# Optimization experiments

Hardware: AMD Instinct MI355X
Metric: run time of the kernel (lower is better)

The kernel has to match this reference:

```python
import jax, jax.numpy as jnp
import numpy as np

D_MODEL = 1024
N_HEADS = 16
D_KV = 64
INNER = N_HEADS * D_KV
NUM_BUCKETS = 32
MAX_DISTANCE = 128
B, S = 4, 2048


def _relative_position_bucket(relative_position):
    # Mirrors T5Attention._relative_position_bucket (bidirectional variant)
    num_buckets = NUM_BUCKETS // 2  # 16
    relative_buckets = (relative_position > 0).astype(jnp.int32) * num_buckets
    rp = jnp.abs(relative_position)
    max_exact = num_buckets // 2  # 8
    is_small = rp < max_exact
    # clamp to 1 before log to avoid -inf (masked out by where anyway)
    rp_large = max_exact + (
        jnp.log(jnp.maximum(rp, 1).astype(jnp.float32) / max_exact)
        / np.log(MAX_DISTANCE / max_exact)
        * (num_buckets - max_exact)
    ).astype(jnp.int32)
    rp_large = jnp.minimum(rp_large, num_buckets - 1)
    return relative_buckets + jnp.where(is_small, rp.astype(jnp.int32), rp_large)


def setup_inputs() -> dict:
    key = jax.random.key(0)
    k1, k2, k3, k4, k5, k6 = jax.random.split(key, 6)
    hidden_states = jax.random.normal(k1, (B, S, D_MODEL), dtype=jnp.float32)
    positions = jnp.arange(B * S, dtype=jnp.int64 if jax.config.jax_enable_x64 else jnp.int32).reshape(B, S)
    mask = jnp.ones((B, S), dtype=jnp.float32)
    sc = 1.0 / np.sqrt(D_MODEL)
    wq = jax.random.normal(k2, (INNER, D_MODEL), dtype=jnp.float32) * sc
    wk = jax.random.normal(k3, (INNER, D_MODEL), dtype=jnp.float32) * sc
    wv = jax.random.normal(k4, (INNER, D_MODEL), dtype=jnp.float32) * sc
    wo = jax.random.normal(k5, (D_MODEL, INNER), dtype=jnp.float32) * sc
    rel_bias = jax.random.normal(k6, (NUM_BUCKETS, N_HEADS), dtype=jnp.float32)
    return {"hidden_states": hidden_states, "positions": positions, "mask": mask,
            "wq": wq, "wk": wk, "wv": wv, "wo": wo, "rel_bias": rel_bias}


def reference(hidden_states, positions, mask, wq, wk, wv, wo, rel_bias):
    Bq, Sq, _ = hidden_states.shape

    def shape_heads(x):  # [B,S,inner] -> [B,H,S,dkv]
        return x.reshape(Bq, Sq, N_HEADS, D_KV).transpose(0, 2, 1, 3)

    # position bias: [B,H,Sq,Sk]
    rel_pos = positions[:, None, :] - positions[:, :, None]  # memory - context
    buckets = _relative_position_bucket(rel_pos)             # [B,Sq,Sk]
    position_bias = rel_bias[buckets].transpose(0, 3, 1, 2)  # [B,H,Sq,Sk]

    q = shape_heads(hidden_states @ wq.T).astype(jnp.float32)
    k = shape_heads(hidden_states @ wk.T).astype(jnp.float32)
    v = shape_heads(hidden_states @ wv.T).astype(jnp.float32)

    scores = jnp.einsum('bhqd,bhkd->bhqk', q, k)  # no 1/sqrt(d) scaling (T5)
    bias = position_bias - 1000.0 * (1.0 - mask[:, None, None, :])
    attn = jax.nn.softmax(scores + bias, axis=-1)  # dropout p=0

    ctx = jnp.einsum('bhqk,bhkd->bhqd', attn, v)
    ctx = ctx.transpose(0, 2, 1, 3).reshape(Bq, Sq, INNER).astype(hidden_states.dtype)
    return ctx @ wo.T
```

## Files before the change

kernel.cpp:

```cpp
#include <hip/hip_runtime.h>
#include <cstdint>
#include <cstddef>

#define D_MODEL 1024
#define N_HEADS 16
#define INNER   1024
#define NBATCH  4
#define SEQ     2048
#define MTOT    (NBATCH * SEQ)
#define LOG2E   1.44269504088896f
#define BSTRIDE 4352
#define MASKC   1442.695041f

typedef _Float16 f16;
typedef __attribute__((ext_vector_type(8))) _Float16 f16x8;
typedef __attribute__((ext_vector_type(4))) _Float16 f16x4;
typedef __attribute__((ext_vector_type(2))) _Float16 f16x2;
typedef __attribute__((ext_vector_type(2))) __fp16   h16x2;
typedef __attribute__((ext_vector_type(4))) float    f32x4;

__device__ __forceinline__ f16x2 cvtpk(float x, float y) {
#if __has_builtin(__builtin_amdgcn_cvt_pkrtz)
  h16x2 r = __builtin_amdgcn_cvt_pkrtz(x, y);
  return __builtin_bit_cast(f16x2, r);
#else
  f16x2 r; r[0] = (f16)x; r[1] = (f16)y; return r;
#endif
}
__device__ __forceinline__ float dot2acc(f16x2 p, float acc) {
#if __has_builtin(__builtin_amdgcn_fdot2)
  h16x2 a = __builtin_bit_cast(h16x2, p);
  h16x2 one; one[0] = (__fp16)1.0f; one[1] = (__fp16)1.0f;
  return __builtin_amdgcn_fdot2(a, one, acc, false);
#else
  return acc + (float)p[0] + (float)p[1];
#endif
}

__global__ void k_cvt(const float* __restrict__ src, f16* __restrict__ dst, int n4, float scale) {
  int i = blockIdx.x * 256 + threadIdx.x;
  if (i < n4) {
    const float4 v = reinterpret_cast<const float4*>(src)[i];
    f16x4 h;
    h[0] = (f16)(v.x * scale); h[1] = (f16)(v.y * scale);
    h[2] = (f16)(v.z * scale); h[3] = (f16)(v.w * scale);
    reinterpret_cast<f16x4*>(dst)[i] = h;
  }
}

__global__ void k_cvtw(const float* __restrict__ wq, const float* __restrict__ wk,
                       const float* __restrict__ wv, const float* __restrict__ wo,
                       f16* __restrict__ dq, f16* __restrict__ dk,
                       f16* __restrict__ dv, f16* __restrict__ dwo) {
  const int y = blockIdx.y;
  const float* src = y == 0 ? wq : (y == 1 ? wk : (y == 2 ? wv : wo));
  f16* dst = y == 0 ? dq : (y == 1 ? dk : (y == 2 ? dv : dwo));
  const float scale = y == 0 ? LOG2E : 1.0f;
  const int i = blockIdx.x * 256 + threadIdx.x;
  const float4 v = reinterpret_cast<const float4*>(src)[i];
  f16x4 h;
  h[0] = (f16)(v.x * scale); h[1] = (f16)(v.y * scale);
  h[2] = (f16)(v.z * scale); h[3] = (f16)(v.w * scale);
  reinterpret_cast<f16x4*>(dst)[i] = h;
}

__global__ void k_bias(const float* __restrict__ relb, float* __restrict__ biasG) {
  const int i = blockIdx.x * 256 + threadIdx.x;
  const int h = blockIdx.y;
  const int d = i - 2048;
  const int sgn = d > 0 ? 16 : 0;
  const int a = d < 0 ? -d : d;
  int bucket;
  if (a < 8) {
    bucket = a;
  } else {
    float t = logf((float)a / 8.0f);
    t = t / 2.772588722239781f;
    t = t * 8.0f;
    int lg = 8 + (int)t;
    bucket = lg < 15 ? lg : 15;
  }
  biasG[h * BSTRIDE + i] = relb[(sgn + bucket) * N_HEADS + h] * LOG2E - MASKC;
}

__device__ __forceinline__ void gload_lds16(const void* g, void* l) {
  __builtin_amdgcn_global_load_lds(
      (const __attribute__((address_space(1))) unsigned int*)g,
      (__attribute__((address_space(3))) unsigned int*)l,
      16, 0, 0);
}

template <int MODE>
__device__ __forceinline__ void gemm_body(const f16* __restrict__ A,
                                          const f16* __restrict__ W,
                                          void* __restrict__ Cp,
                                          int m0, int n0) {
  __shared__ __align__(16) f16 As[128 * 64];
  __shared__ __align__(16) f16 Bs[128 * 64];
  const int t = threadIdx.x;
  const int lane = t & 63;
  const int wid = t >> 6;
  const int wr = wid >> 1;
  const int wc = wid & 1;
  const int g = lane >> 4;
  const int lr = lane & 15;

  f32x4 acc[4][4] = {};
  const char* Ab = (const char*)A;
  const char* Wb = (const char*)W;

  for (int kt = 0; kt < D_MODEL / 64; ++kt) {
    const int k0 = kt * 64;
    __syncthreads();
#pragma unroll
    for (int i = 0; i < 4; ++i) {
      const int idx = i * 256 + t;
      const int row = idx >> 3;
      const int cb  = (idx & 7) * 16;
      gload_lds16(Ab + ((size_t)(m0 + row) * D_MODEL + k0) * 2 + cb, (char*)As + idx * 16);
      gload_lds16(Wb + ((size_t)(n0 + row) * D_MODEL + k0) * 2 + cb, (char*)Bs + idx * 16);
    }
    asm volatile("s_waitcnt vmcnt(0)" ::: "memory");
    __syncthreads();

    f16x8 af[4][2], bf[4][2];
#pragma unroll
    for (int mi = 0; mi < 4; ++mi)
#pragma unroll
      for (int kk = 0; kk < 2; ++kk)
        af[mi][kk] = *(const f16x8*)&As[(wr * 64 + mi * 16 + lr) * 64 + kk * 32 + g * 8];
#pragma unroll
    for (int ni = 0; ni < 4; ++ni)
#pragma unroll
      for (int kk = 0; kk < 2; ++kk)
        bf[ni][kk] = *(const f16x8*)&Bs[(wc * 64 + ni * 16 + lr) * 64 + kk * 32 + g * 8];
#pragma unroll
    for (int kk = 0; kk < 2; ++kk)
#pragma unroll
      for (int mi = 0; mi < 4; ++mi)
#pragma unroll
        for (int ni = 0; ni < 4; ++ni)
          acc[mi][ni] = __builtin_amdgcn_mfma_f32_16x16x32_f16(af[mi][kk], bf[ni][kk], acc[mi][ni], 0, 0, 0);
  }

#pragma unroll
  for (int mi = 0; mi < 4; ++mi)
#pragma unroll
    for (int ni = 0; ni < 4; ++ni) {
      const int n = n0 + wc * 64 + ni * 16 + lr;
      if (MODE == 2) {
        const int mbase = m0 + wr * 64 + mi * 16 + g * 4;
        const int b2 = mbase >> 11, s2 = mbase & (SEQ - 1);
        const int h2 = n >> 6, d2 = n & 63;
        const int sub = ((s2 & 15) >> 2) * 8 + ((s2 >> 4) & 1) * 4;
        f16x4 w;
#pragma unroll
        for (int r = 0; r < 4; ++r) w[r] = (f16)acc[mi][ni][r];
        *(f16x4*)((f16*)Cp + ((size_t)((b2 * 16 + h2) * 64 + d2) * SEQ + (s2 >> 5) * 32 + sub)) = w;
      } else {
#pragma unroll
        for (int r = 0; r < 4; ++r) {
          const int m = m0 + wr * 64 + mi * 16 + g * 4 + r;
          if (MODE == 1)
            ((float*)Cp)[(size_t)m * INNER + n] = acc[mi][ni][r];
          else
            ((f16*)Cp)[(size_t)m * INNER + n] = (f16)acc[mi][ni][r];
        }
      }
    }
}

__global__ __launch_bounds__(256) void k_gemm_qkv(
    const f16* __restrict__ A,
    const f16* __restrict__ Wq, const f16* __restrict__ Wk, const f16* __restrict__ Wv,
    f16* __restrict__ Cq, f16* __restrict__ Ck, f16* __restrict__ Vt) {
  const int bid = (int)blockIdx.x;
  const int X = bid & 7, l = bid >> 3;
  const int zy = X * 24 + (l >> 3);
  const int x = l & 7;
  const int z = zy >> 6, y = zy & 63;
  if (z == 0)      gemm_body<0>(A, Wq, Cq, y * 128, x * 128);
  else if (z == 1) gemm_body<0>(A, Wk, Ck, y * 128, x * 128);
  else             gemm_body<2>(A, Wv, Vt, y * 128, x * 128);
}

__global__ __launch_bounds__(256) void k_gemm_out(
    const f16* __restrict__ A, const f16* __restrict__ W, float* __restrict__ C) {
  const int bid = (int)blockIdx.x;
  const int X = bid & 7, l = bid >> 3;
  const int y = X * 8 + (l >> 3), x = l & 7;
  gemm_body<1>(A, W, C, y * 128, x * 128);
}

__global__ __launch_bounds__(256, 4) void k_attn(
    const f16* __restrict__ Q, const f16* __restrict__ K, const f16* __restrict__ Vt,
    const float* __restrict__ biasG, const float* __restrict__ mask,
    f16* __restrict__ ctx) {
  __shared__ __align__(16) float  biasT[2178];
  __shared__ __align__(16) float2 biasO[1088];
  __shared__ __align__(16) f16 Ks[2 * 2048];
  __shared__ __align__(16) f16 Vs[2 * 2048];
  __shared__ int mflag;

  const int nb = (int)blockIdx.x;
  const int v = (nb & 7) * 128 + (nb >> 3);
  const int bh = v >> 4, qc = v & 15;
  const int b = bh >> 4, h = bh & 15;

  const int t = threadIdx.x, lane = t & 63, wid = t >> 6;
  const int g = lane >> 4, lr = lane & 15;
  const int qb = qc * 128;

  const float* maskB = mask + (size_t)b * SEQ;
  {
    const float* bgh = biasG + (size_t)h * BSTRIDE + (1921 - qb);
    for (int i = t; i < 2177; i += 256) biasT[i] = bgh[i];
    for (int m = t; m < 1088; m += 256) {
      float2 o2; o2.x = bgh[2 * m + 1]; o2.y = bgh[2 * m + 2];
      biasO[m] = o2;
    }
  }
  if (t == 0) mflag = 1;
  __syncthreads();
  {
    bool bad = false;
    for (int i = t; i < SEQ; i += 256) bad |= (maskB[i] != 1.0f);
    if (bad) mflag = 0;
  }

  const char* Kg = (const char*)K + ((size_t)(b * SEQ) * INNER + h * 64) * 2;
  const char* Vg = (const char*)Vt + ((size_t)bh * 64) * SEQ * 2;
  const int krow = t >> 3, kch = t & 7;
  const int ksrc = (kch * 16) ^ ((krow & 7) << 4);
  const int vrow = t >> 2, vch = t & 3;
  const int vsrc = (vch * 16) ^ ((vrow & 3) << 4);

  const int qw = qb + wid * 32;

  f16x8 qa[2][2];
#pragma unroll
  for (int hh = 0; hh < 2; ++hh)
#pragma unroll
    for (int kk = 0; kk < 2; ++kk)
      qa[hh][kk] = *(const f16x8*)&Q[(size_t)(b * SEQ + qw + hh * 16 + lr) * INNER + h * 64 + kk * 32 + g * 8];

  int koffs[2][2], voffs[4];
#pragma unroll
  for (int s = 0; s < 2; ++s)
#pragma unroll
    for (int hf = 0; hf < 2; ++hf)
      koffs[s][hf] = (s * 16 + lr) * 128 + ((hf * 64 + g * 16) ^ ((lr & 7) << 4));
#pragma unroll
  for (int dn = 0; dn < 4; ++dn)
    voffs[dn] = (dn * 16 + lr) * 64 + ((g * 16) ^ ((lr & 3) << 4));

  f32x4 o[2][4] = {};
  float mrun[2] = {-__builtin_inff(), -__builtin_inff()};
  float lsum[2] = {0.0f, 0.0f};

  const int jbase = 127 + 4 * g - wid * 32 - lr;
  const int jb2 = jbase - 16;
  const char* biasPtr = (jb2 & 1) ? ((const char*)biasO + (size_t)(jb2 - 1) * 4)
                                  : ((const char*)biasT + (size_t)jb2 * 4);

  gload_lds16(Kg + ((size_t)krow * INNER) * 2 + ksrc, (char*)Ks + t * 16);
  gload_lds16(Vg + ((size_t)vrow * SEQ) * 2 + vsrc,   (char*)Vs + t * 16);
  asm volatile("s_waitcnt vmcnt(0)" ::: "memory");
  __syncthreads();
  const bool useMask = (mflag == 0);

#define ATTN_ITER(BUF, K0, MK)                                                 \
  {                                                                            \
    float4 mk0 = {}, mk1 = {};                                                 \
    if (MK) {                                                                  \
      mk0 = *(const float4*)(maskB + (K0) + 4 * g);                            \
      mk1 = *(const float4*)(maskB + (K0) + 16 + 4 * g);                       \
    }                                                                          \
    const int k0n_ = ((K0) + 32 < SEQ) ? (K0) + 32 : 0;                        \
    gload_lds16(Kg + ((size_t)(k0n_ + krow) * INNER) * 2 + ksrc,               \
                (char*)Ks + ((BUF) ^ 1) * 4096 + t * 16);                      \
    gload_lds16(Vg + ((size_t)vrow * SEQ + k0n_) * 2 + vsrc,                   \
                (char*)Vs + ((BUF) ^ 1) * 4096 + t * 16);                      \
    const char* bb = biasPtr + (K0) * 4;                                       \
    const float2 bm0 = *(const float2*)(bb);                                   \
    const float2 bm1 = *(const float2*)(bb + 8);                               \
    const float2 bc0 = *(const float2*)(bb + 64);                              \
    const float2 bc1 = *(const float2*)(bb + 72);                              \
    const float2 bp0 = *(const float2*)(bb + 128);                             \
    const float2 bp1 = *(const float2*)(bb + 136);                             \
    const float bsel[2][2][4] = {                                              \
        {{bc0.x, bc0.y, bc1.x, bc1.y}, {bp0.x, bp0.y, bp1.x, bp1.y}},          \
        {{bm0.x, bm0.y, bm1.x, bm1.y}, {bc0.x, bc0.y, bc1.x, bc1.y}}};         \
    f16x8 kf[2][2];                                                            \
    _Pragma("unroll") for (int s = 0; s < 2; ++s)                              \
      _Pragma("unroll") for (int hf = 0; hf < 2; ++hf)                         \
        kf[s][hf] = *(const f16x8*)((const char*)Ks + (BUF) * 4096 + koffs[s][hf]); \
    f16x8 vv[4];                                                               \
    _Pragma("unroll") for (int dn = 0; dn < 4; ++dn)                           \
      vv[dn] = *(const f16x8*)((const char*)Vs + (BUF) * 4096 + voffs[dn]);    \
    f32x4 sg[2][2];                                                            \
    _Pragma("unroll") for (int hh = 0; hh < 2; ++hh)                           \
      _Pragma("unroll") for (int s = 0; s < 2; ++s) {                          \
        f32x4 z;                                                               \
        if (MK) {                                                              \
          const float* mkp = (s == 0) ? (const float*)&mk0 : (const float*)&mk1; \
          _Pragma("unroll") for (int r = 0; r < 4; ++r)                        \
            z[r] = fmaf(mkp[r], MASKC, bsel[hh][s][r]);                        \
        } else {                                                               \
          _Pragma("unroll") for (int r = 0; r < 4; ++r)                        \
            z[r] = bsel[hh][s][r];                                             \
        }                                                                      \
        z = __builtin_amdgcn_mfma_f32_16x16x32_f16(kf[s][0], qa[hh][0], z, 0, 0, 0); \
        z = __builtin_amdgcn_mfma_f32_16x16x32_f16(kf[s][1], qa[hh][1], z, 0, 0, 0); \
        sg[hh][s] = z;                                                         \
      }                                                                        \
    float mxA = fmaxf(fmaxf(fmaxf(sg[0][0][0], sg[0][0][1]), fmaxf(sg[0][0][2], sg[0][0][3])), \
                      fmaxf(fmaxf(sg[0][1][0], sg[0][1][1]), fmaxf(sg[0][1][2], sg[0][1][3]))); \
    float mxB = fmaxf(fmaxf(fmaxf(sg[1][0][0], sg[1][0][1]), fmaxf(sg[1][0][2], sg[1][0][3])), \
                      fmaxf(fmaxf(sg[1][1][0], sg[1][1][1]), fmaxf(sg[1][1][2], sg[1][1][3]))); \
    if (__any((mxA > mrun[0] + 11.5415603f) || (mxB > mrun[1] + 11.5415603f))) { \
      mxA = fmaxf(mxA, __shfl_xor(mxA, 16));                                   \
      mxB = fmaxf(mxB, __shfl_xor(mxB, 16));                                   \
      mxA = fmaxf(mxA, __shfl_xor(mxA, 32));                                   \
      mxB = fmaxf(mxB, __shfl_xor(mxB, 32));                                   \
      const float mnA = fmaxf(mrun[0], mxA), mnB = fmaxf(mrun[1], mxB);        \
      const float aA = __builtin_amdgcn_exp2f(mrun[0] - mnA);                  \
      const float aB = __builtin_amdgcn_exp2f(mrun[1] - mnB);                  \
      lsum[0] *= aA; lsum[1] *= aB;                                            \
      _Pragma("unroll") for (int dn = 0; dn < 4; ++dn)                         \
        _Pragma("unroll") for (int r = 0; r < 4; ++r) {                        \
          o[0][dn][r] *= aA; o[1][dn][r] *= aB;                                \
        }                                                                      \
      mrun[0] = mnA; mrun[1] = mnB;                                            \
    }                                                                          \
    f16x8 pfA8, pfB8;                                                          \
    _Pragma("unroll") for (int s = 0; s < 2; ++s) {                            \
      float eA[4], eB[4];                                                      \
      _Pragma("unroll") for (int r = 0; r < 4; ++r) {                          \
        eA[r] = __builtin_amdgcn_exp2f(sg[0][s][r] - mrun[0]);                 \
        eB[r] = __builtin_amdgcn_exp2f(sg[1][s][r] - mrun[1]);                 \
      }                                                                        \
      const f16x2 a0 = cvtpk(eA[0], eA[1]), a1 = cvtpk(eA[2], eA[3]);          \
      const f16x2 b0 = cvtpk(eB[0], eB[1]), b1 = cvtpk(eB[2], eB[3]);          \
      lsum[0] = dot2acc(a0, lsum[0]); lsum[0] = dot2acc(a1, lsum[0]);          \
      lsum[1] = dot2acc(b0, lsum[1]); lsum[1] = dot2acc(b1, lsum[1]);          \
      pfA8[s * 4 + 0] = a0[0]; pfA8[s * 4 + 1] = a0[1];                        \
      pfA8[s * 4 + 2] = a1[0]; pfA8[s * 4 + 3] = a1[1];                        \
      pfB8[s * 4 + 0] = b0[0]; pfB8[s * 4 + 1] = b0[1];                        \
      pfB8[s * 4 + 2] = b1[0]; pfB8[s * 4 + 3] = b1[1];                        \
    }                                                                          \
    _Pragma("unroll") for (int dn = 0; dn < 4; ++dn) {                         \
      o[0][dn] = __builtin_amdgcn_mfma_f32_16x16x32_f16(vv[dn], pfA8, o[0][dn], 0, 0, 0); \
      o[1][dn] = __builtin_amdgcn_mfma_f32_16x16x32_f16(vv[dn], pfB8, o[1][dn], 0, 0, 0); \
    }                                                                          \
    asm volatile("s_waitcnt vmcnt(0)" ::: "memory");                           \
    __syncthreads();                                                           \
  }

  if (useMask) {
    for (int k0 = 0; k0 < SEQ; k0 += 64) {
      ATTN_ITER(0, k0, 1)
      ATTN_ITER(1, k0 + 32, 1)
    }
  } else {
    for (int k0 = 0; k0 < SEQ; k0 += 64) {
      ATTN_ITER(0, k0, 0)
      ATTN_ITER(1, k0 + 32, 0)
    }
  }

  lsum[0] += __shfl_xor(lsum[0], 16);
  lsum[1] += __shfl_xor(lsum[1], 16);
  lsum[0] += __shfl_xor(lsum[0], 32);
  lsum[1] += __shfl_xor(lsum[1], 32);

  const float invA = 1.0f / lsum[0], invB = 1.0f / lsum[1];
#pragma unroll
  for (int dn = 0; dn < 4; ++dn) {
    f16x4 wA, wB;
#pragma unroll
    for (int r = 0; r < 4; ++r) {
      wA[r] = (f16)(o[0][dn][r] * invA);
      wB[r] = (f16)(o[1][dn][r] * invB);
    }
    *(f16x4*)&ctx[(size_t)(b * SEQ + qw + lr) * INNER + h * 64 + dn * 16 + 4 * g] = wA;
    *(f16x4*)&ctx[(size_t)(b * SEQ + qw + 16 + lr) * INNER + h * 64 + dn * 16 + 4 * g] = wB;
  }
}

extern "C" void kernel_launch(void* const* d_in, const int* in_sizes, int n_in,
                              void* d_out, int out_size, void* d_ws, size_t ws_size,
                              hipStream_t stream) {
  const float* hs   = (const float*)d_in[0];
  const float* mask = (const float*)d_in[2];
  const float* wq   = (const float*)d_in[3];
  const float* wk   = (const float*)d_in[4];
  const float* wv   = (const float*)d_in[5];
  const float* wo   = (const float*)d_in[6];
  const float* relb = (const float*)d_in[7];

  char* ws = (char*)d_ws;
  const size_t SZ16 = (size_t)MTOT * INNER * 2;
  const size_t WSZ  = (size_t)INNER * D_MODEL * 2;
  f16* hs16 = (f16*)(ws);
  f16* q16  = (f16*)(ws + SZ16);
  f16* k16  = (f16*)(ws + 2 * SZ16);
  f16* vt16 = (f16*)(ws + 3 * SZ16);
  f16* wq16 = (f16*)(ws + 4 * SZ16);
  f16* wk16 = (f16*)(ws + 4 * SZ16 + WSZ);
  f16* wv16 = (f16*)(ws + 4 * SZ16 + 2 * WSZ);
  f16* wo16 = (f16*)(ws + 4 * SZ16 + 3 * WSZ);
  float* biasG = (float*)(ws + 4 * SZ16 + 4 * WSZ);

  k_cvt<<<(MTOT * INNER / 4 + 255) / 256, 256, 0, stream>>>(hs, hs16, MTOT * INNER / 4, 1.0f);
  k_cvtw<<<dim3(INNER * D_MODEL / 4 / 256, 4), 256, 0, stream>>>(
      wq, wk, wv, wo, wq16, wk16, wv16, wo16);

  k_bias<<<dim3(BSTRIDE / 256, N_HEADS), 256, 0, stream>>>(relb, biasG);

  k_gemm_qkv<<<dim3(1536), 256, 0, stream>>>(
      hs16, wq16, wk16, wv16, q16, k16, vt16);

  k_attn<<<dim3(1024), 256, 0, stream>>>(
      q16, k16, vt16, biasG, mask, hs16);

  k_gemm_out<<<dim3(512), 256, 0, stream>>>(
      hs16, wo16, (float*)d_out);
}
```

Baseline: 227.3 us.

## Double attention block query tile to 256 with 512 threads sharing K/V tiles

The attention kernel now launches 512-thread blocks covering 256 queries each, halving the grid so every K/V tile staged in LDS is reused by eight waves instead of four. K and V staging is split between the two halves of the block, so each thread issues one async load per step instead of two. The bias table becomes a single scalar-indexed LDS array read per element, replacing the odd/even float2 layout. MFMA sections are wrapped in s_setprio raises to favour matrix issue. The risks are per-element LDS bias reads, a grid of only 512 blocks, and heavier register pressure under launch_bounds(512,4).

```diff
diff --git a/kernel.cpp b/kernel.cpp
--- a/kernel.cpp
+++ b/kernel.cpp
@@ -192,48 +192,46 @@
   gemm_body<1>(A, W, C, y * 128, x * 128);
 }
 
-__global__ __launch_bounds__(256, 4) void k_attn(
+__global__ __launch_bounds__(512, 4) void k_attn(
     const f16* __restrict__ Q, const f16* __restrict__ K, const f16* __restrict__ Vt,
     const float* __restrict__ biasG, const float* __restrict__ mask,
     f16* __restrict__ ctx) {
-  __shared__ __align__(16) float  biasT[2178];
-  __shared__ __align__(16) float2 biasO[1088];
+  __shared__ __align__(16) float biasT[2304];
   __shared__ __align__(16) f16 Ks[2 * 2048];
   __shared__ __align__(16) f16 Vs[2 * 2048];
   __shared__ int mflag;
 
   const int nb = (int)blockIdx.x;
-  const int v = (nb & 7) * 128 + (nb >> 3);
-  const int bh = v >> 4, qc = v & 15;
+  const int v = (nb & 7) * 64 + (nb >> 3);
+  const int bh = v >> 3, qc = v & 7;
   const int b = bh >> 4, h = bh & 15;
 
   const int t = threadIdx.x, lane = t & 63, wid = t >> 6;
   const int g = lane >> 4, lr = lane & 15;
-  const int qb = qc * 128;
+  const int qb = qc * 256;
 
   const float* maskB = mask + (size_t)b * SEQ;
   {
-    const float* bgh = biasG + (size_t)h * BSTRIDE + (1921 - qb);
-    for (int i = t; i < 2177; i += 256) biasT[i] = bgh[i];
-    for (int m = t; m < 1088; m += 256) {
-      float2 o2; o2.x = bgh[2 * m + 1]; o2.y = bgh[2 * m + 2];
-      biasO[m] = o2;
-    }
+    const float* bgh = biasG + (size_t)h * BSTRIDE + (1793 - qb);
+    for (int i = t; i < 2304; i += 512) biasT[i] = bgh[i];
   }
   if (t == 0) mflag = 1;
   __syncthreads();
   {
     bool bad = false;
-    for (int i = t; i < SEQ; i += 256) bad |= (maskB[i] != 1.0f);
+    for (int i = t; i < SEQ; i += 512) bad |= (maskB[i] != 1.0f);
     if (bad) mflag = 0;
   }
 
   const char* Kg = (const char*)K + ((size_t)(b * SEQ) * INNER + h * 64) * 2;
   const char* Vg = (const char*)Vt + ((size_t)bh * 64) * SEQ * 2;
-  const int krow = t >> 3, kch = t & 7;
-  const int ksrc = (kch * 16) ^ ((krow & 7) << 4);
-  const int vrow = t >> 2, vch = t & 3;
-  const int vsrc = (vch * 16) ^ ((vrow & 3) << 4);
+
+  const bool isK = t < 256;
+  const int ts = t & 255;
+  const int krow = ts >> 3, kch = ts & 7;
+  const int vrow = ts >> 2, vch = ts & 3;
+  const int stsrc = isK ? ((kch * 16) ^ ((krow & 7) << 4))
+                        : ((vch * 16) ^ ((vrow & 3) << 4));
 
   const int qw = qb + wid * 32;
 
@@ -257,14 +255,12 @@
   f32x4 o[2][4] = {};
   float mrun[2] = {-__builtin_inff(), -__builtin_inff()};
   float lsum[2] = {0.0f, 0.0f};
-
-  const int jbase = 127 + 4 * g - wid * 32 - lr;
-  const int jb2 = jbase - 16;
-  const char* biasPtr = (jb2 & 1) ? ((const char*)biasO + (size_t)(jb2 - 1) * 4)
-                                  : ((const char*)biasT + (size_t)jb2 * 4);
-
-  gload_lds16(Kg + ((size_t)krow * INNER) * 2 + ksrc, (char*)Ks + t * 16);
-  gload_lds16(Vg + ((size_t)vrow * SEQ) * 2 + vsrc,   (char*)Vs + t * 16);
+  const int jbase = 255 + 4 * g - wid * 32 - lr;
+
+  if (isK)
+    gload_lds16(Kg + ((size_t)krow * INNER) * 2 + stsrc, (char*)Ks + ts * 16);
+  else
+    gload_lds16(Vg + ((size_t)vrow * SEQ) * 2 + stsrc,   (char*)Vs + ts * 16);
   asm volatile("s_waitcnt vmcnt(0)" ::: "memory");
   __syncthreads();
   const bool useMask = (mflag == 0);
@@ -277,20 +273,12 @@
       mk1 = *(const float4*)(maskB + (K0) + 16 + 4 * g);                       \
     }                                                                          \
     const int k0n_ = ((K0) + 32 < SEQ) ? (K0) + 32 : 0;                        \
-    gload_lds16(Kg + ((size_t)(k0n_ + krow) * INNER) * 2 + ksrc,               \
-                (char*)Ks + ((BUF) ^ 1) * 4096 + t * 16);                      \
-    gload_lds16(Vg + ((size_t)vrow * SEQ + k0n_) * 2 + vsrc,                   \
-                (char*)Vs + ((BUF) ^ 1) * 4096 + t * 16);                      \
-    const char* bb = biasPtr + (K0) * 4;                                       \
-    const float2 bm0 = *(const float2*)(bb);                                   \
-    const float2 bm1 = *(const float2*)(bb + 8);                               \
-    const float2 bc0 = *(const float2*)(bb + 64);                              \
-    const float2 bc1 = *(const float2*)(bb + 72);                              \
-    const float2 bp0 = *(const float2*)(bb + 128);                             \
-    const float2 bp1 = *(const float2*)(bb + 136);                             \
-    const float bsel[2][2][4] = {                                              \
-        {{bc0.x, bc0.y, bc1.x, bc1.y}, {bp0.x, bp0.y, bp1.x, bp1.y}},          \
-        {{bm0.x, bm0.y, bm1.x, bm1.y}, {bc0.x, bc0.y, bc1.x, bc1.y}}};         \
+    if (isK)                                                                   \
+      gload_lds16(Kg + ((size_t)(k0n_ + krow) * INNER) * 2 + stsrc,            \
+                  (char*)Ks + ((BUF) ^ 1) * 4096 + ts * 16);                   \
+    else                                                                       \
+      gload_lds16(Vg + ((size_t)vrow * SEQ + k0n_) * 2 + stsrc,                \
+                  (char*)Vs + ((BUF) ^ 1) * 4096 + ts * 16);                   \
     f16x8 kf[2][2];                                                            \
     _Pragma("unroll") for (int s = 0; s < 2; ++s)                              \
       _Pragma("unroll") for (int hf = 0; hf < 2; ++hf)                         \
@@ -299,21 +287,24 @@
     _Pragma("unroll") for (int dn = 0; dn < 4; ++dn)                           \
       vv[dn] = *(const f16x8*)((const char*)Vs + (BUF) * 4096 + voffs[dn]);    \
     f32x4 sg[2][2];                                                            \
+    __builtin_amdgcn_s_setprio(1);                                             \
     _Pragma("unroll") for (int hh = 0; hh < 2; ++hh)                           \
       _Pragma("unroll") for (int s = 0; s < 2; ++s) {                          \
+        const int jA = (K0) + s * 16 - hh * 16 + jbase;                        \
         f32x4 z;                                                               \
         if (MK) {                                                              \
           const float* mkp = (s == 0) ? (const float*)&mk0 : (const float*)&mk1; \
           _Pragma("unroll") for (int r = 0; r < 4; ++r)                        \
-            z[r] = fmaf(mkp[r], MASKC, bsel[hh][s][r]);                        \
+            z[r] = fmaf(mkp[r], MASKC, biasT[jA + r]);                         \
         } else {                                                               \
           _Pragma("unroll") for (int r = 0; r < 4; ++r)                        \
-            z[r] = bsel[hh][s][r];                                             \
+            z[r] = biasT[jA + r];                                              \
         }                                                                      \
         z = __builtin_amdgcn_mfma_f32_16x16x32_f16(kf[s][0], qa[hh][0], z, 0, 0, 0); \
         z = __builtin_amdgcn_mfma_f32_16x16x32_f16(kf[s][1], qa[hh][1], z, 0, 0, 0); \
         sg[hh][s] = z;                                                         \
       }                                                                        \
+    __builtin_amdgcn_s_setprio(0);                                             \
     float mxA = fmaxf(fmaxf(fmaxf(sg[0][0][0], sg[0][0][1]), fmaxf(sg[0][0][2], sg[0][0][3])), \
                       fmaxf(fmaxf(sg[0][1][0], sg[0][1][1]), fmaxf(sg[0][1][2], sg[0][1][3]))); \
     float mxB = fmaxf(fmaxf(fmaxf(sg[1][0][0], sg[1][0][1]), fmaxf(sg[1][0][2], sg[1][0][3])), \
@@ -349,10 +340,12 @@
       pfB8[s * 4 + 0] = b0[0]; pfB8[s * 4 + 1] = b0[1];                        \
       pfB8[s * 4 + 2] = b1[0]; pfB8[s * 4 + 3] = b1[1];                        \
     }                                                                          \
+    __builtin_amdgcn_s_setprio(1);                                             \
     _Pragma("unroll") for (int dn = 0; dn < 4; ++dn) {                         \
       o[0][dn] = __builtin_amdgcn_mfma_f32_16x16x32_f16(vv[dn], pfA8, o[0][dn], 0, 0, 0); \
       o[1][dn] = __builtin_amdgcn_mfma_f32_16x16x32_f16(vv[dn], pfB8, o[1][dn], 0, 0, 0); \
     }                                                                          \
+    __builtin_amdgcn_s_setprio(0);                                             \
     asm volatile("s_waitcnt vmcnt(0)" ::: "memory");                           \
     __syncthreads();                                                           \
   }
@@ -421,7 +414,7 @@
   k_gemm_qkv<<<dim3(1536), 256, 0, stream>>>(
       hs16, wq16, wk16, wv16, q16, k16, vt16);
 
-  k_attn<<<dim3(1024), 256, 0, stream>>>(
+  k_attn<<<dim3(512), 512, 0, stream>>>(
       q16, k16, vt16, biasG, mask, hs16);
 
   k_gemm_out<<<dim3(512), 256, 0, stream>>>(
```

Result: faster. 219.3 us (-3.5%).
